# Optimization experiments

Hardware: AMD Instinct MI355X
Metric: run time of the kernel (lower is better)

The kernel has to match this reference:

```python
import jax, jax.numpy as jnp
import numpy as np

B, L, H, Q = 64, 512, 1024, 64
VA_H = 256


def setup_inputs() -> dict:
    key = jax.random.key(0)
    ks = jax.random.split(key, 10)
    hidden_states = jax.random.normal(ks[0], (B, L, H), dtype=jnp.float32)
    quad_spans = jax.random.randint(ks[1], (B, Q, 4), 0, L, dtype=jnp.int64)
    quad_mask = jnp.ones((B, Q), dtype=jnp.int32)
    s = 0.02
    W1 = jax.random.normal(ks[2], (3 * H, VA_H), dtype=jnp.float32) * s
    b1 = jnp.zeros((VA_H,), dtype=jnp.float32)
    W2 = jax.random.normal(ks[3], (VA_H, VA_H // 2), dtype=jnp.float32) * s
    b2 = jnp.zeros((VA_H // 2,), dtype=jnp.float32)
    W3 = jax.random.normal(ks[4], (VA_H // 2, 2), dtype=jnp.float32) * s
    b3 = jnp.zeros((2,), dtype=jnp.float32)
    return {"hidden_states": hidden_states, "quad_spans": quad_spans,
            "quad_mask": quad_mask, "W1": W1, "b1": b1, "W2": W2, "b2": b2,
            "W3": W3, "b3": b3}


def _pool_spans(hidden_states, quad_spans, quad_mask):
    # hidden_states [B,L,H]; quad_spans [B,Q,4]; quad_mask [B,Q]
    Bn, Ln, Hn = hidden_states.shape
    pos = jnp.arange(Ln)[None, None, :]                      # [1,1,L]
    asp_s = quad_spans[:, :, 0:1]
    asp_e = quad_spans[:, :, 1:2]
    opi_s = quad_spans[:, :, 2:3]
    opi_e = quad_spans[:, :, 3:4]
    asp_valid = asp_s >= 2
    opi_valid = opi_s >= 2
    sep = pos == 1                                           # [SEP] fallback
    asp_m = ((pos >= asp_s) & (pos <= asp_e) & asp_valid) | (~asp_valid & sep)
    opi_m = ((pos >= opi_s) & (pos <= opi_e) & opi_valid) | (~opi_valid & sep)
    qm = (quad_mask != 0)[:, :, None]
    asp_f = (asp_m & qm).astype(hidden_states.dtype)         # [B,Q,L]
    opi_f = (opi_m & qm).astype(hidden_states.dtype)
    h_asp = jnp.einsum('bql,blh->bqh', asp_f, hidden_states) / jnp.clip(
        asp_f.sum(-1, keepdims=True), 1.0, None)
    h_opi = jnp.einsum('bql,blh->bqh', opi_f, hidden_states) / jnp.clip(
        opi_f.sum(-1, keepdims=True), 1.0, None)
    return h_asp, h_opi


def reference(hidden_states, quad_spans, quad_mask, W1, b1, W2, b2, W3, b3):
    h_asp, h_opi = _pool_spans(hidden_states, quad_spans, quad_mask)
    h_pair = jnp.concatenate([h_asp, h_opi, h_asp * h_opi], axis=-1)  # [B,Q,3H]
    x = jax.nn.gelu(h_pair @ W1 + b1, approximate=False)   # torch GELU = exact
    x = jax.nn.gelu(x @ W2 + b2, approximate=False)        # dropout: eval mode
    x = x @ W3 + b3                                        # [B,Q,2]
    va = jax.nn.sigmoid(x) * 8.0 + 1.0
    return va * quad_mask[:, :, None].astype(va.dtype)
```

## Files before the change

### kernel.cpp

```cpp
#include <hip/hip_runtime.h>
#include <math.h>


typedef __attribute__((ext_vector_type(4))) float f32x4;
typedef __attribute__((ext_vector_type(8))) short bf16x8;

#define NPAIR 4096
#define LSEQ 512
#define HDIM 1024

#if defined(__has_builtin)
#if __has_builtin(__builtin_amdgcn_global_load_lds)
#define HAVE_GLDS 1
#endif
#endif
#ifndef HAVE_GLDS
#define HAVE_GLDS 0
#endif

__device__ __forceinline__ unsigned int pack2(float lo, float hi) {
  const unsigned int a = __float_as_uint(lo) + 0x8000u;
  const unsigned int b = __float_as_uint(hi) + 0x8000u;
  return __builtin_amdgcn_perm(b, a, 0x07060302u);
}
__device__ __forceinline__ unsigned short f2bf(float f) {
  return (unsigned short)((__float_as_uint(f) + 0x8000u) >> 16);
}
__device__ __forceinline__ float gelu(float x) {
  return 0.5f * x * (1.f + erff(x * 0.70710678118654752f));
}

__global__ __launch_bounds__(256, 4) void prep_kernel(
    const float* __restrict__ hs, const int* __restrict__ spans,
    const int* __restrict__ qmask, unsigned short* __restrict__ hpair,
    const float* __restrict__ W1, unsigned short* __restrict__ W1T,
    const float* __restrict__ W2, unsigned short* __restrict__ W2T) {
  __shared__ __align__(16) unsigned char smem[34816];
  __shared__ float scl[128];
  const int tid = threadIdx.x;

  if (blockIdx.x >= 1024) {
    float(*t)[33] = (float(*)[33])smem;
    const float* in;
    unsigned short* out;
    int C, R, c0, r0;
    int blk = blockIdx.x - 1024;
    if (blk < 768) {
      in = W1; out = W1T; R = 3072; C = 256;
      c0 = (blk & 7) * 32; r0 = (blk >> 3) * 32;
    } else {
      blk -= 768;
      in = W2; out = W2T; R = 256; C = 128;
      c0 = (blk & 3) * 32; r0 = (blk >> 2) * 32;
    }
    const int x = tid & 31, y = tid >> 5;
#pragma unroll
    for (int i = 0; i < 32; i += 8)
      t[y + i][x] = in[(size_t)(r0 + y + i) * C + c0 + x];
    __syncthreads();
#pragma unroll
    for (int i = 0; i < 32; i += 8)
      out[(size_t)(c0 + y + i) * R + r0 + x] = f2bf(t[x][y + i]);
    return;
  }

  typedef unsigned short BlT[64][40];
  BlT* Bl = (BlT*)smem;
  float(*S)[68] = (float(*)[68])smem;

  const int b = blockIdx.x >> 4;
  const int n0 = (blockIdx.x & 15) * 64;
  const int lane = tid & 63;
  const int lm = lane & 15, quad = lane >> 4;
  const int wm = (tid >> 6) * 32;

  const bool is64 =
      (spans[1] == 0) && (spans[3] == 0) && (spans[5] == 0) && (spans[7] == 0);

  auto span_of = [&](int r, int& s, int& e) {
    const int q = r & 63, t = r >> 6;
    const int idx = (b * 64 + q) * 4 + t * 2;
    s = is64 ? spans[idx * 2] : spans[idx];
    e = is64 ? spans[idx * 2 + 2] : spans[idx + 1];
    if (s < 2) { s = 1; e = 1; }
  };
  int s0, e0, s1, e1;
  span_of(wm + lm, s0, e0);
  span_of(wm + 16 + lm, s1, e1);

  if (tid < 128) {
    int s, e;
    span_of(tid, s, e);
    const int c = (e >= s) ? (e - s + 1) : 0;
    const float sc = 1.f / (float)(c < 1 ? 1 : c);
    scl[tid] = (qmask[b * 64 + (tid & 63)] != 0) ? sc : 0.f;
  }

  f32x4 acc[2][4];
#pragma unroll
  for (int f = 0; f < 2; ++f)
#pragma unroll
    for (int g = 0; g < 4; ++g) acc[f][g] = f32x4{0.f, 0.f, 0.f, 0.f};

  const float* hsb = hs + (size_t)b * (LSEQ * HDIM);
  const int nl = tid & 63;
  const int kw = (tid >> 6) * 8;

  auto load8 = [&](int kbase, unsigned int (&tmp)[4]) {
    const float* src = hsb + (size_t)(kbase + kw) * HDIM + n0 + nl;
#pragma unroll
    for (int i = 0; i < 4; ++i) {
      const float f0 = src[(size_t)(2 * i) * HDIM];
      const float f1 = src[(size_t)(2 * i + 1) * HDIM];
      tmp[i] = pack2(f0, f1);
    }
  };

  unsigned int tmp[4];
  load8(0, tmp);
  *(uint4*)&Bl[0][nl][kw] = make_uint4(tmp[0], tmp[1], tmp[2], tmp[3]);

  for (int it = 0; it < 16; ++it) {
    const int k0 = it * 32;
    __syncthreads();
    if (it < 15) load8(k0 + 32, tmp);

    bf16x8 a0, a1;
#pragma unroll
    for (int j = 0; j < 8; ++j) {
      const int k = k0 + quad * 8 + j;
      a0[j] = (short)((k >= s0 && k <= e0) ? 0x3F80 : 0);
      a1[j] = (short)((k >= s1 && k <= e1) ? 0x3F80 : 0);
    }
    const BlT& Bc = Bl[it & 1];
#pragma unroll
    for (int g = 0; g < 4; ++g) {
      bf16x8 bg = *(const bf16x8*)&Bc[g * 16 + lm][quad * 8];
      acc[0][g] = __builtin_amdgcn_mfma_f32_16x16x32_bf16(a0, bg, acc[0][g], 0, 0, 0);
      acc[1][g] = __builtin_amdgcn_mfma_f32_16x16x32_bf16(a1, bg, acc[1][g], 0, 0, 0);
    }
    if (it < 15) {
      *(uint4*)&Bl[(it + 1) & 1][nl][kw] = make_uint4(tmp[0], tmp[1], tmp[2], tmp[3]);
    }
  }

  __syncthreads();
#pragma unroll
  for (int f = 0; f < 2; ++f)
#pragma unroll
    for (int g = 0; g < 4; ++g)
#pragma unroll
      for (int r = 0; r < 4; ++r)
        S[wm + f * 16 + quad * 4 + r][g * 16 + lm] = acc[f][g][r];
  __syncthreads();

  const int q = tid >> 2;
  const int cg = (tid & 3) * 16;
  const float sA = scl[q], sO = scl[64 + q];
  unsigned short* dst = hpair + (size_t)(b * 64 + q) * 3072 + n0 + cg;
#pragma unroll
  for (int h = 0; h < 2; ++h) {
    float a[8], o[8];
#pragma unroll
    for (int i = 0; i < 8; ++i) {
      a[i] = S[q][cg + h * 8 + i] * sA;
      o[i] = S[64 + q][cg + h * 8 + i] * sO;
    }
    uint4 wa, wo, wp;
    wa.x = pack2(a[0], a[1]); wa.y = pack2(a[2], a[3]);
    wa.z = pack2(a[4], a[5]); wa.w = pack2(a[6], a[7]);
    wo.x = pack2(o[0], o[1]); wo.y = pack2(o[2], o[3]);
    wo.z = pack2(o[4], o[5]); wo.w = pack2(o[6], o[7]);
    wp.x = pack2(a[0] * o[0], a[1] * o[1]); wp.y = pack2(a[2] * o[2], a[3] * o[3]);
    wp.z = pack2(a[4] * o[4], a[5] * o[5]); wp.w = pack2(a[6] * o[6], a[7] * o[7]);
    *(uint4*)(dst + h * 8) = wa;
    *(uint4*)(dst + 1024 + h * 8) = wo;
    *(uint4*)(dst + 2048 + h * 8) = wp;
  }
}

__global__ __launch_bounds__(256) void gemm_bt_64x256(
    const unsigned short* __restrict__ A, const unsigned short* __restrict__ Bt,
    float* __restrict__ P, int M, int N, int K, int KH) {
  __shared__ __align__(16) unsigned short Al[2][64][32];
  __shared__ __align__(16) unsigned short Bl[2][256][32];
  const int bm = blockIdx.x * 64;
  const int kz = blockIdx.z * KH;
  const int tid = threadIdx.x;
  const int wave = tid >> 6, lane = tid & 63;
  const int wn = wave * 64;
  const int lm = lane & 15, lk = (lane >> 4) * 8;

  const int srow = lane >> 2;
  const int scol = (lane & 3) * 8;
  const unsigned short* ga = A + (size_t)(bm + wave * 16 + srow) * K + kz + scol;
  const unsigned short* gb = Bt + (size_t)(wn + srow) * K + kz + scol;

  f32x4 acc[4][4];
#pragma unroll
  for (int i = 0; i < 4; ++i)
#pragma unroll
    for (int j = 0; j < 4; ++j) acc[i][j] = f32x4{0.f, 0.f, 0.f, 0.f};

  auto stage = [&](int u, int k0) {
#if HAVE_GLDS
    __builtin_amdgcn_global_load_lds(ga + k0, &Al[u][wave * 16][0], 16, 0, 0);
#pragma unroll
    for (int c = 0; c < 4; ++c)
      __builtin_amdgcn_global_load_lds(gb + (size_t)(c * 16) * K + k0,
                                       &Bl[u][wn + c * 16][0], 16, 0, 0);
#else
    *(uint4*)&Al[u][wave * 16 + srow][scol] = *(const uint4*)(ga + k0);
#pragma unroll
    for (int c = 0; c < 4; ++c)
      *(uint4*)&Bl[u][wn + c * 16 + srow][scol] =
          *(const uint4*)(gb + (size_t)(c * 16) * K + k0);
#endif
  };

  const int NT = KH / 32;
  stage(0, 0);
  for (int t = 0; t < NT; ++t) {
    __syncthreads();
    if (t + 1 < NT) stage((t + 1) & 1, (t + 1) * 32);
    const int u = t & 1;
    bf16x8 af[4], bf[4];
#pragma unroll
    for (int i = 0; i < 4; ++i) {
      af[i] = *(const bf16x8*)&Al[u][i * 16 + lm][lk];
      bf[i] = *(const bf16x8*)&Bl[u][wn + i * 16 + lm][lk];
    }
#pragma unroll
    for (int i = 0; i < 4; ++i)
#pragma unroll
      for (int j = 0; j < 4; ++j)
        acc[i][j] = __builtin_amdgcn_mfma_f32_16x16x32_bf16(af[i], bf[j], acc[i][j], 0, 0, 0);
  }

  float* Pz = P + (size_t)blockIdx.z * M * N;
  const int rq = (lane >> 4) << 2;
#pragma unroll
  for (int i = 0; i < 4; ++i)
#pragma unroll
    for (int j = 0; j < 4; ++j) {
      const int r0 = bm + i * 16 + rq;
      const int c0 = wn + j * 16 + lm;
#pragma unroll
      for (int r = 0; r < 4; ++r)
        Pz[(size_t)(r0 + r) * N + c0] = acc[i][j][r];
    }
}

__global__ __launch_bounds__(256) void tail_kernel(
    const float* __restrict__ P, const float* __restrict__ b1,
    const unsigned short* __restrict__ W2T, const float* __restrict__ b2,
    const float* __restrict__ W3, const float* __restrict__ b3,
    const int* __restrict__ qmask, float* __restrict__ out) {
  __shared__ __align__(16) unsigned short Al[16 * 264];
  __shared__ float S2[16][132];
  __shared__ float w3[256];

  const int m0 = blockIdx.x * 16;
  const int tid = threadIdx.x;
  const int wave = tid >> 6, lane = tid & 63;
  const int lm = lane & 15, quad = lane >> 4;
  const int wn = wave * 32;

  w3[tid] = W3[tid];

  {
    const int row = tid >> 4;
    const int slot = tid & 15;
#pragma unroll
    for (int ss = 0; ss < 2; ++ss) {
      const int s = slot + ss * 16;
      const float* pb = P + (size_t)(m0 + row) * 256 + s * 8;
      float v[8];
      {
        float4 ba = *(const float4*)(b1 + s * 8);
        float4 bb = *(const float4*)(b1 + s * 8 + 4);
        v[0] = ba.x; v[1] = ba.y; v[2] = ba.z; v[3] = ba.w;
        v[4] = bb.x; v[5] = bb.y; v[6] = bb.z; v[7] = bb.w;
      }
#pragma unroll
      for (int z = 0; z < 4; ++z) {
        const float* pz = pb + (size_t)z * ((size_t)NPAIR * 256);
        float4 a0 = *(const float4*)pz;
        float4 a1 = *(const float4*)(pz + 4);
        v[0] += a0.x; v[1] += a0.y; v[2] += a0.z; v[3] += a0.w;
        v[4] += a1.x; v[5] += a1.y; v[6] += a1.z; v[7] += a1.w;
      }
      uint4 w;
      w.x = pack2(gelu(v[0]), gelu(v[1]));
      w.y = pack2(gelu(v[2]), gelu(v[3]));
      w.z = pack2(gelu(v[4]), gelu(v[5]));
      w.w = pack2(gelu(v[6]), gelu(v[7]));
      *(uint4*)((char*)Al + (size_t)row * 528 + s * 16) = w;
    }
  }
  __syncthreads();

  f32x4 acc[2];
  acc[0] = f32x4{0.f, 0.f, 0.f, 0.f};
  acc[1] = f32x4{0.f, 0.f, 0.f, 0.f};
#pragma unroll
  for (int ks = 0; ks < 8; ++ks) {
    bf16x8 a = *(const bf16x8*)((char*)Al + (size_t)lm * 528 + ks * 64 + quad * 16);
#pragma unroll
    for (int g = 0; g < 2; ++g) {
      const int n = wn + g * 16 + lm;
      bf16x8 b = *(const bf16x8*)(W2T + (size_t)n * 256 + ks * 32 + quad * 8);
      acc[g] = __builtin_amdgcn_mfma_f32_16x16x32_bf16(a, b, acc[g], 0, 0, 0);
    }
  }

#pragma unroll
  for (int g = 0; g < 2; ++g) {
    const int col = wn + g * 16 + lm;
    const float bc = b2[col];
#pragma unroll
    for (int r = 0; r < 4; ++r) S2[quad * 4 + r][col] = gelu(acc[g][r] + bc);
  }
  __syncthreads();

  if (tid < 128) {
    const int row = tid >> 3, o = (tid >> 2) & 1, q4 = tid & 3;
    float part = 0.f;
#pragma unroll 8
    for (int c = q4; c < 128; c += 4) part += S2[row][c] * w3[c * 2 + o];
    part += __shfl_xor(part, 1);
    part += __shfl_xor(part, 2);
    if (q4 == 0) {
      const int pair = m0 + row;
      const float a = part + b3[o];
      const float qmf = (float)qmask[pair];
      out[pair * 2 + o] = ((1.f / (1.f + expf(-a))) * 8.f + 1.f) * qmf;
    }
  }
}

extern "C" void kernel_launch(void* const* d_in, const int* in_sizes, int n_in,
                              void* d_out, int out_size, void* d_ws,
                              size_t ws_size, hipStream_t stream) {
  const float* hs = (const float*)d_in[0];
  const int* spans = (const int*)d_in[1];
  const int* qmask = (const int*)d_in[2];
  const float* W1 = (const float*)d_in[3];
  const float* b1 = (const float*)d_in[4];
  const float* W2 = (const float*)d_in[5];
  const float* b2 = (const float*)d_in[6];
  const float* W3 = (const float*)d_in[7];
  const float* b3 = (const float*)d_in[8];
  float* out = (float*)d_out;

  const size_t HPAIR_B = 25165824;
  const size_t P_B = 16777216;
  const size_t W1T_B = 1572864;

  char* ws = (char*)d_ws;
  size_t off = 0;
  unsigned short* hpair = (unsigned short*)(ws + off); off += HPAIR_B;
  float* P = (float*)(ws + off);                       off += P_B;
  unsigned short* W1T = (unsigned short*)(ws + off);   off += W1T_B;
  unsigned short* W2T = (unsigned short*)(ws + off);

  prep_kernel<<<1824, 256, 0, stream>>>(hs, spans, qmask, hpair, W1, W1T, W2, W2T);
  gemm_bt_64x256<<<dim3(64, 1, 4), 256, 0, stream>>>(hpair, W1T, P, NPAIR,
                                                     256, 3072, 768);
  tail_kernel<<<256, 256, 0, stream>>>(P, b1, W2T, b2, W3, b3, qmask, out);
}
```

Baseline: 238.9 us.

## Fuse split-K GEMM and MLP tail into one kernel with atomic counters

Merges the split-K W1 GEMM and the tail MLP kernel into a single launch of 256 blocks. Each group of four K-split blocks signals completion through a per-row-tile atomic counter, which prep_kernel resets. Each block then spins until its group finishes and reduces its own 16-row slice. This removes one kernel launch and the gap between kernels. In exchange it relies on all blocks of a group being co-resident, since the spin-wait would deadlock otherwise, and adds fence and atomic overhead.

```diff
diff --git a/kernel.cpp b/kernel.cpp
--- a/kernel.cpp
+++ b/kernel.cpp
@@ -34,12 +34,14 @@
     const float* __restrict__ hs, const int* __restrict__ spans,
     const int* __restrict__ qmask, unsigned short* __restrict__ hpair,
     const float* __restrict__ W1, unsigned short* __restrict__ W1T,
-    const float* __restrict__ W2, unsigned short* __restrict__ W2T) {
+    const float* __restrict__ W2, unsigned short* __restrict__ W2T,
+    unsigned int* __restrict__ cnt) {
   __shared__ __align__(16) unsigned char smem[34816];
   __shared__ float scl[128];
   const int tid = threadIdx.x;
 
   if (blockIdx.x >= 1024) {
+    if (blockIdx.x == 1024 && tid < 64) cnt[tid] = 0;
     float(*t)[33] = (float(*)[33])smem;
     const float* in;
     unsigned short* out;
@@ -179,94 +181,111 @@
   }
 }
 
-__global__ __launch_bounds__(256) void gemm_bt_64x256(
+__global__ __launch_bounds__(256) void gemm_tail_kernel(
     const unsigned short* __restrict__ A, const unsigned short* __restrict__ Bt,
-    float* __restrict__ P, int M, int N, int K, int KH) {
-  __shared__ __align__(16) unsigned short Al[2][64][32];
-  __shared__ __align__(16) unsigned short Bl[2][256][32];
-  const int bm = blockIdx.x * 64;
-  const int kz = blockIdx.z * KH;
-  const int tid = threadIdx.x;
-  const int wave = tid >> 6, lane = tid & 63;
-  const int wn = wave * 64;
-  const int lm = lane & 15, lk = (lane >> 4) * 8;
-
-  const int srow = lane >> 2;
-  const int scol = (lane & 3) * 8;
-  const unsigned short* ga = A + (size_t)(bm + wave * 16 + srow) * K + kz + scol;
-  const unsigned short* gb = Bt + (size_t)(wn + srow) * K + kz + scol;
-
-  f32x4 acc[4][4];
-#pragma unroll
-  for (int i = 0; i < 4; ++i)
-#pragma unroll
-    for (int j = 0; j < 4; ++j) acc[i][j] = f32x4{0.f, 0.f, 0.f, 0.f};
-
-  auto stage = [&](int u, int k0) {
-#if HAVE_GLDS
-    __builtin_amdgcn_global_load_lds(ga + k0, &Al[u][wave * 16][0], 16, 0, 0);
-#pragma unroll
-    for (int c = 0; c < 4; ++c)
-      __builtin_amdgcn_global_load_lds(gb + (size_t)(c * 16) * K + k0,
-                                       &Bl[u][wn + c * 16][0], 16, 0, 0);
-#else
-    *(uint4*)&Al[u][wave * 16 + srow][scol] = *(const uint4*)(ga + k0);
-#pragma unroll
-    for (int c = 0; c < 4; ++c)
-      *(uint4*)&Bl[u][wn + c * 16 + srow][scol] =
-          *(const uint4*)(gb + (size_t)(c * 16) * K + k0);
-#endif
-  };
-
-  const int NT = KH / 32;
-  stage(0, 0);
-  for (int t = 0; t < NT; ++t) {
-    __syncthreads();
-    if (t + 1 < NT) stage((t + 1) & 1, (t + 1) * 32);
-    const int u = t & 1;
-    bf16x8 af[4], bf[4];
-#pragma unroll
-    for (int i = 0; i < 4; ++i) {
-      af[i] = *(const bf16x8*)&Al[u][i * 16 + lm][lk];
-      bf[i] = *(const bf16x8*)&Bl[u][wn + i * 16 + lm][lk];
-    }
-#pragma unroll
-    for (int i = 0; i < 4; ++i)
-#pragma unroll
-      for (int j = 0; j < 4; ++j)
-        acc[i][j] = __builtin_amdgcn_mfma_f32_16x16x32_bf16(af[i], bf[j], acc[i][j], 0, 0, 0);
-  }
-
-  float* Pz = P + (size_t)blockIdx.z * M * N;
-  const int rq = (lane >> 4) << 2;
-#pragma unroll
-  for (int i = 0; i < 4; ++i)
-#pragma unroll
-    for (int j = 0; j < 4; ++j) {
-      const int r0 = bm + i * 16 + rq;
-      const int c0 = wn + j * 16 + lm;
-#pragma unroll
-      for (int r = 0; r < 4; ++r)
-        Pz[(size_t)(r0 + r) * N + c0] = acc[i][j][r];
-    }
-}
-
-__global__ __launch_bounds__(256) void tail_kernel(
-    const float* __restrict__ P, const float* __restrict__ b1,
+    float* __restrict__ P, const float* __restrict__ b1,
     const unsigned short* __restrict__ W2T, const float* __restrict__ b2,
     const float* __restrict__ W3, const float* __restrict__ b3,
-    const int* __restrict__ qmask, float* __restrict__ out) {
-  __shared__ __align__(16) unsigned short Al[16 * 264];
-  __shared__ float S2[16][132];
-  __shared__ float w3[256];
-
-  const int m0 = blockIdx.x * 16;
+    const int* __restrict__ qmask, float* __restrict__ out,
+    unsigned int* __restrict__ cnt) {
+  __shared__ __align__(16) unsigned char smem[40960];
   const int tid = threadIdx.x;
   const int wave = tid >> 6, lane = tid & 63;
   const int lm = lane & 15, quad = lane >> 4;
-  const int wn = wave * 32;
-
+
+  const int m = blockIdx.x >> 2, z = blockIdx.x & 3;
+  const int K = 3072, N = 256, KH = 768;
+
+  {
+    typedef unsigned short AlT[64][32];
+    typedef unsigned short BlT[256][32];
+    AlT* Al = (AlT*)smem;
+    BlT* Bl = (BlT*)(smem + 8192);
+    const int bm = m * 64;
+    const int kz = z * KH;
+    const int wn = wave * 64;
+    const int lk = (lane >> 4) * 8;
+
+    const int srow = lane >> 2;
+    const int scol = (lane & 3) * 8;
+    const unsigned short* ga = A + (size_t)(bm + wave * 16 + srow) * K + kz + scol;
+    const unsigned short* gb = Bt + (size_t)(wn + srow) * K + kz + scol;
+
+    f32x4 acc[4][4];
+#pragma unroll
+    for (int i = 0; i < 4; ++i)
+#pragma unroll
+      for (int j = 0; j < 4; ++j) acc[i][j] = f32x4{0.f, 0.f, 0.f, 0.f};
+
+    auto stage = [&](int u, int k0) {
+#if HAVE_GLDS
+      __builtin_amdgcn_global_load_lds(ga + k0, &Al[u][wave * 16][0], 16, 0, 0);
+#pragma unroll
+      for (int c = 0; c < 4; ++c)
+        __builtin_amdgcn_global_load_lds(gb + (size_t)(c * 16) * K + k0,
+                                         &Bl[u][wn + c * 16][0], 16, 0, 0);
+#else
+      *(uint4*)&Al[u][wave * 16 + srow][scol] = *(const uint4*)(ga + k0);
+#pragma unroll
+      for (int c = 0; c < 4; ++c)
+        *(uint4*)&Bl[u][wn + c * 16 + srow][scol] =
+            *(const uint4*)(gb + (size_t)(c * 16) * K + k0);
+#endif
+    };
+
+    const int NT = KH / 32;
+    stage(0, 0);
+    for (int t = 0; t < NT; ++t) {
+      __syncthreads();
+      if (t + 1 < NT) stage((t + 1) & 1, (t + 1) * 32);
+      const int u = t & 1;
+      bf16x8 af[4], bf[4];
+#pragma unroll
+      for (int i = 0; i < 4; ++i) {
+        af[i] = *(const bf16x8*)&Al[u][i * 16 + lm][lk];
+        bf[i] = *(const bf16x8*)&Bl[u][wn + i * 16 + lm][lk];
+      }
+#pragma unroll
+      for (int i = 0; i < 4; ++i)
+#pragma unroll
+        for (int j = 0; j < 4; ++j)
+          acc[i][j] = __builtin_amdgcn_mfma_f32_16x16x32_bf16(af[i], bf[j], acc[i][j], 0, 0, 0);
+    }
+
+    float* Pz = P + (size_t)z * NPAIR * N;
+    const int rq = (lane >> 4) << 2;
+#pragma unroll
+    for (int i = 0; i < 4; ++i)
+#pragma unroll
+      for (int j = 0; j < 4; ++j) {
+        const int r0 = bm + i * 16 + rq;
+        const int c0 = wn + j * 16 + lm;
+#pragma unroll
+        for (int r = 0; r < 4; ++r)
+          Pz[(size_t)(r0 + r) * N + c0] = acc[i][j][r];
+      }
+  }
+
+  __threadfence();
+  __syncthreads();
+  unsigned short* Ax = (unsigned short*)smem;
+  float(*S2)[132] = (float(*)[132])(smem + 8448);
+  float* w3 = (float*)(smem + 16896);
   w3[tid] = W3[tid];
+
+  if (tid == 0) {
+    __hip_atomic_fetch_add(&cnt[m], 1u, __ATOMIC_RELEASE,
+                           __HIP_MEMORY_SCOPE_AGENT);
+    while (__hip_atomic_load(&cnt[m], __ATOMIC_ACQUIRE,
+                             __HIP_MEMORY_SCOPE_AGENT) < 4u) {
+      __builtin_amdgcn_s_sleep(8);
+    }
+  }
+  __syncthreads();
+  (void)__hip_atomic_load(&cnt[m], __ATOMIC_ACQUIRE, __HIP_MEMORY_SCOPE_AGENT);
+
+  const int m0 = blockIdx.x * 16;
+  const int wn2 = wave * 32;
 
   {
     const int row = tid >> 4;
@@ -283,8 +302,8 @@
         v[4] = bb.x; v[5] = bb.y; v[6] = bb.z; v[7] = bb.w;
       }
 #pragma unroll
-      for (int z = 0; z < 4; ++z) {
-        const float* pz = pb + (size_t)z * ((size_t)NPAIR * 256);
+      for (int zz = 0; zz < 4; ++zz) {
+        const float* pz = pb + (size_t)zz * ((size_t)NPAIR * 256);
         float4 a0 = *(const float4*)pz;
         float4 a1 = *(const float4*)(pz + 4);
         v[0] += a0.x; v[1] += a0.y; v[2] += a0.z; v[3] += a0.w;
@@ -295,31 +314,31 @@
       w.y = pack2(gelu(v[2]), gelu(v[3]));
       w.z = pack2(gelu(v[4]), gelu(v[5]));
       w.w = pack2(gelu(v[6]), gelu(v[7]));
-      *(uint4*)((char*)Al + (size_t)row * 528 + s * 16) = w;
-    }
-  }
-  __syncthreads();
-
-  f32x4 acc[2];
-  acc[0] = f32x4{0.f, 0.f, 0.f, 0.f};
-  acc[1] = f32x4{0.f, 0.f, 0.f, 0.f};
+      *(uint4*)((char*)Ax + (size_t)row * 528 + s * 16) = w;
+    }
+  }
+  __syncthreads();
+
+  f32x4 acc2[2];
+  acc2[0] = f32x4{0.f, 0.f, 0.f, 0.f};
+  acc2[1] = f32x4{0.f, 0.f, 0.f, 0.f};
 #pragma unroll
   for (int ks = 0; ks < 8; ++ks) {
-    bf16x8 a = *(const bf16x8*)((char*)Al + (size_t)lm * 528 + ks * 64 + quad * 16);
+    bf16x8 a = *(const bf16x8*)((char*)Ax + (size_t)lm * 528 + ks * 64 + quad * 16);
 #pragma unroll
     for (int g = 0; g < 2; ++g) {
-      const int n = wn + g * 16 + lm;
+      const int n = wn2 + g * 16 + lm;
       bf16x8 b = *(const bf16x8*)(W2T + (size_t)n * 256 + ks * 32 + quad * 8);
-      acc[g] = __builtin_amdgcn_mfma_f32_16x16x32_bf16(a, b, acc[g], 0, 0, 0);
+      acc2[g] = __builtin_amdgcn_mfma_f32_16x16x32_bf16(a, b, acc2[g], 0, 0, 0);
     }
   }
 
 #pragma unroll
   for (int g = 0; g < 2; ++g) {
-    const int col = wn + g * 16 + lm;
+    const int col = wn2 + g * 16 + lm;
     const float bc = b2[col];
 #pragma unroll
-    for (int r = 0; r < 4; ++r) S2[quad * 4 + r][col] = gelu(acc[g][r] + bc);
+    for (int r = 0; r < 4; ++r) S2[quad * 4 + r][col] = gelu(acc2[g][r] + bc);
   }
   __syncthreads();
 
@@ -356,16 +375,18 @@
   const size_t HPAIR_B = 25165824;
   const size_t P_B = 16777216;
   const size_t W1T_B = 1572864;
+  const size_t W2T_B = 65536;
 
   char* ws = (char*)d_ws;
   size_t off = 0;
   unsigned short* hpair = (unsigned short*)(ws + off); off += HPAIR_B;
   float* P = (float*)(ws + off);                       off += P_B;
   unsigned short* W1T = (unsigned short*)(ws + off);   off += W1T_B;
-  unsigned short* W2T = (unsigned short*)(ws + off);
-
-  prep_kernel<<<1824, 256, 0, stream>>>(hs, spans, qmask, hpair, W1, W1T, W2, W2T);
-  gemm_bt_64x256<<<dim3(64, 1, 4), 256, 0, stream>>>(hpair, W1T, P, NPAIR,
-                                                     256, 3072, 768);
-  tail_kernel<<<256, 256, 0, stream>>>(P, b1, W2T, b2, W3, b3, qmask, out);
-}
+  unsigned short* W2T = (unsigned short*)(ws + off);   off += W2T_B;
+  unsigned int* cnt = (unsigned int*)(ws + off);
+
+  prep_kernel<<<1824, 256, 0, stream>>>(hs, spans, qmask, hpair, W1, W1T, W2,
+                                        W2T, cnt);
+  gemm_tail_kernel<<<256, 256, 0, stream>>>(hpair, W1T, P, b1, W2T, b2, W3,
+                                            b3, qmask, out, cnt);
+}
```

Result: slower. 270.9 us (+13.4%).

## Fuse first-layer GEMM into MLP tail kernel, drop split-K partial buffer

Applied to the files above, without the earlier changes.

Replaces the split-K LDS-staged W1 GEMM and the separate tail kernel with one kernel. Each 512-thread block computes 16 rows across all 256 hidden columns, loading A and W1T fragments straight from global memory into registers, then applies GELU and runs the W2/W3 stages in the same block. This removes the 16 MB fp32 partial-sum buffer, its write and read-back, and one launch. The cost is no LDS reuse: every wave reloads the same A rows, and W1T is read by all 256 blocks, so only 256 blocks stream the full K=3072 with less reuse than the tiled GEMM.

```diff
diff --git a/kernel.cpp b/kernel.cpp
--- a/kernel.cpp
+++ b/kernel.cpp
@@ -8,15 +8,6 @@
 #define NPAIR 4096
 #define LSEQ 512
 #define HDIM 1024
-
-#if defined(__has_builtin)
-#if __has_builtin(__builtin_amdgcn_global_load_lds)
-#define HAVE_GLDS 1
-#endif
-#endif
-#ifndef HAVE_GLDS
-#define HAVE_GLDS 0
-#endif
 
 __device__ __forceinline__ unsigned int pack2(float lo, float hi) {
   const unsigned int a = __float_as_uint(lo) + 0x8000u;
@@ -179,147 +170,74 @@
   }
 }
 
-__global__ __launch_bounds__(256) void gemm_bt_64x256(
-    const unsigned short* __restrict__ A, const unsigned short* __restrict__ Bt,
-    float* __restrict__ P, int M, int N, int K, int KH) {
-  __shared__ __align__(16) unsigned short Al[2][64][32];
-  __shared__ __align__(16) unsigned short Bl[2][256][32];
-  const int bm = blockIdx.x * 64;
-  const int kz = blockIdx.z * KH;
-  const int tid = threadIdx.x;
-  const int wave = tid >> 6, lane = tid & 63;
-  const int wn = wave * 64;
-  const int lm = lane & 15, lk = (lane >> 4) * 8;
-
-  const int srow = lane >> 2;
-  const int scol = (lane & 3) * 8;
-  const unsigned short* ga = A + (size_t)(bm + wave * 16 + srow) * K + kz + scol;
-  const unsigned short* gb = Bt + (size_t)(wn + srow) * K + kz + scol;
-
-  f32x4 acc[4][4];
-#pragma unroll
-  for (int i = 0; i < 4; ++i)
-#pragma unroll
-    for (int j = 0; j < 4; ++j) acc[i][j] = f32x4{0.f, 0.f, 0.f, 0.f};
-
-  auto stage = [&](int u, int k0) {
-#if HAVE_GLDS
-    __builtin_amdgcn_global_load_lds(ga + k0, &Al[u][wave * 16][0], 16, 0, 0);
-#pragma unroll
-    for (int c = 0; c < 4; ++c)
-      __builtin_amdgcn_global_load_lds(gb + (size_t)(c * 16) * K + k0,
-                                       &Bl[u][wn + c * 16][0], 16, 0, 0);
-#else
-    *(uint4*)&Al[u][wave * 16 + srow][scol] = *(const uint4*)(ga + k0);
-#pragma unroll
-    for (int c = 0; c < 4; ++c)
-      *(uint4*)&Bl[u][wn + c * 16 + srow][scol] =
-          *(const uint4*)(gb + (size_t)(c * 16) * K + k0);
-#endif
-  };
-
-  const int NT = KH / 32;
-  stage(0, 0);
-  for (int t = 0; t < NT; ++t) {
-    __syncthreads();
-    if (t + 1 < NT) stage((t + 1) & 1, (t + 1) * 32);
-    const int u = t & 1;
-    bf16x8 af[4], bf[4];
-#pragma unroll
-    for (int i = 0; i < 4; ++i) {
-      af[i] = *(const bf16x8*)&Al[u][i * 16 + lm][lk];
-      bf[i] = *(const bf16x8*)&Bl[u][wn + i * 16 + lm][lk];
-    }
-#pragma unroll
-    for (int i = 0; i < 4; ++i)
-#pragma unroll
-      for (int j = 0; j < 4; ++j)
-        acc[i][j] = __builtin_amdgcn_mfma_f32_16x16x32_bf16(af[i], bf[j], acc[i][j], 0, 0, 0);
-  }
-
-  float* Pz = P + (size_t)blockIdx.z * M * N;
-  const int rq = (lane >> 4) << 2;
-#pragma unroll
-  for (int i = 0; i < 4; ++i)
-#pragma unroll
-    for (int j = 0; j < 4; ++j) {
-      const int r0 = bm + i * 16 + rq;
-      const int c0 = wn + j * 16 + lm;
-#pragma unroll
-      for (int r = 0; r < 4; ++r)
-        Pz[(size_t)(r0 + r) * N + c0] = acc[i][j][r];
-    }
-}
-
-__global__ __launch_bounds__(256) void tail_kernel(
-    const float* __restrict__ P, const float* __restrict__ b1,
-    const unsigned short* __restrict__ W2T, const float* __restrict__ b2,
-    const float* __restrict__ W3, const float* __restrict__ b3,
-    const int* __restrict__ qmask, float* __restrict__ out) {
-  __shared__ __align__(16) unsigned short Al[16 * 264];
+__global__ __launch_bounds__(512) void mlp_kernel(
+    const unsigned short* __restrict__ A, const unsigned short* __restrict__ W1T,
+    const float* __restrict__ b1, const unsigned short* __restrict__ W2T,
+    const float* __restrict__ b2, const float* __restrict__ W3,
+    const float* __restrict__ b3, const int* __restrict__ qmask,
+    float* __restrict__ out) {
+  __shared__ __align__(16) unsigned short x1[16 * 264];
   __shared__ float S2[16][132];
   __shared__ float w3[256];
 
-  const int m0 = blockIdx.x * 16;
+  const int bm = blockIdx.x * 16;
   const int tid = threadIdx.x;
   const int wave = tid >> 6, lane = tid & 63;
   const int lm = lane & 15, quad = lane >> 4;
-  const int wn = wave * 32;
-
-  w3[tid] = W3[tid];
+
+  if (tid < 256) w3[tid] = W3[tid];
+
+  const int wn1 = wave * 32;
+  const unsigned short* pa = A + (size_t)(bm + lm) * 3072 + quad * 8;
+  const unsigned short* pb0 = W1T + (size_t)(wn1 + lm) * 3072 + quad * 8;
+  const unsigned short* pb1 = W1T + (size_t)(wn1 + 16 + lm) * 3072 + quad * 8;
+
+  f32x4 acc1[2];
+  acc1[0] = f32x4{0.f, 0.f, 0.f, 0.f};
+  acc1[1] = f32x4{0.f, 0.f, 0.f, 0.f};
+
+  for (int kb = 0; kb < 3072; kb += 256) {
+    bf16x8 av[8], b0v[8], b1v[8];
+#pragma unroll
+    for (int s = 0; s < 8; ++s) {
+      const int k0 = kb + s * 32;
+      av[s] = *(const bf16x8*)(pa + k0);
+      b0v[s] = *(const bf16x8*)(pb0 + k0);
+      b1v[s] = *(const bf16x8*)(pb1 + k0);
+    }
+#pragma unroll
+    for (int s = 0; s < 8; ++s) {
+      acc1[0] = __builtin_amdgcn_mfma_f32_16x16x32_bf16(av[s], b0v[s], acc1[0], 0, 0, 0);
+      acc1[1] = __builtin_amdgcn_mfma_f32_16x16x32_bf16(av[s], b1v[s], acc1[1], 0, 0, 0);
+    }
+  }
+
+#pragma unroll
+  for (int g = 0; g < 2; ++g) {
+    const int n = wn1 + g * 16 + lm;
+    const float bc = b1[n];
+#pragma unroll
+    for (int r = 0; r < 4; ++r) {
+      x1[(quad * 4 + r) * 264 + n] = f2bf(gelu(acc1[g][r] + bc));
+    }
+  }
+  __syncthreads();
+
+  const int wn2 = wave * 16;
+  f32x4 acc2 = f32x4{0.f, 0.f, 0.f, 0.f};
+  const unsigned short* pw2 = W2T + (size_t)(wn2 + lm) * 256 + quad * 8;
+#pragma unroll
+  for (int ks = 0; ks < 8; ++ks) {
+    bf16x8 a = *(const bf16x8*)&x1[lm * 264 + ks * 32 + quad * 8];
+    bf16x8 b = *(const bf16x8*)(pw2 + ks * 32);
+    acc2 = __builtin_amdgcn_mfma_f32_16x16x32_bf16(a, b, acc2, 0, 0, 0);
+  }
 
   {
-    const int row = tid >> 4;
-    const int slot = tid & 15;
-#pragma unroll
-    for (int ss = 0; ss < 2; ++ss) {
-      const int s = slot + ss * 16;
-      const float* pb = P + (size_t)(m0 + row) * 256 + s * 8;
-      float v[8];
-      {
-        float4 ba = *(const float4*)(b1 + s * 8);
-        float4 bb = *(const float4*)(b1 + s * 8 + 4);
-        v[0] = ba.x; v[1] = ba.y; v[2] = ba.z; v[3] = ba.w;
-        v[4] = bb.x; v[5] = bb.y; v[6] = bb.z; v[7] = bb.w;
-      }
-#pragma unroll
-      for (int z = 0; z < 4; ++z) {
-        const float* pz = pb + (size_t)z * ((size_t)NPAIR * 256);
-        float4 a0 = *(const float4*)pz;
-        float4 a1 = *(const float4*)(pz + 4);
-        v[0] += a0.x; v[1] += a0.y; v[2] += a0.z; v[3] += a0.w;
-        v[4] += a1.x; v[5] += a1.y; v[6] += a1.z; v[7] += a1.w;
-      }
-      uint4 w;
-      w.x = pack2(gelu(v[0]), gelu(v[1]));
-      w.y = pack2(gelu(v[2]), gelu(v[3]));
-      w.z = pack2(gelu(v[4]), gelu(v[5]));
-      w.w = pack2(gelu(v[6]), gelu(v[7]));
-      *(uint4*)((char*)Al + (size_t)row * 528 + s * 16) = w;
-    }
-  }
-  __syncthreads();
-
-  f32x4 acc[2];
-  acc[0] = f32x4{0.f, 0.f, 0.f, 0.f};
-  acc[1] = f32x4{0.f, 0.f, 0.f, 0.f};
-#pragma unroll
-  for (int ks = 0; ks < 8; ++ks) {
-    bf16x8 a = *(const bf16x8*)((char*)Al + (size_t)lm * 528 + ks * 64 + quad * 16);
-#pragma unroll
-    for (int g = 0; g < 2; ++g) {
-      const int n = wn + g * 16 + lm;
-      bf16x8 b = *(const bf16x8*)(W2T + (size_t)n * 256 + ks * 32 + quad * 8);
-      acc[g] = __builtin_amdgcn_mfma_f32_16x16x32_bf16(a, b, acc[g], 0, 0, 0);
-    }
-  }
-
-#pragma unroll
-  for (int g = 0; g < 2; ++g) {
-    const int col = wn + g * 16 + lm;
+    const int col = wn2 + lm;
     const float bc = b2[col];
 #pragma unroll
-    for (int r = 0; r < 4; ++r) S2[quad * 4 + r][col] = gelu(acc[g][r] + bc);
+    for (int r = 0; r < 4; ++r) S2[quad * 4 + r][col] = gelu(acc2[r] + bc);
   }
   __syncthreads();
 
@@ -331,7 +249,7 @@
     part += __shfl_xor(part, 1);
     part += __shfl_xor(part, 2);
     if (q4 == 0) {
-      const int pair = m0 + row;
+      const int pair = bm + row;
       const float a = part + b3[o];
       const float qmf = (float)qmask[pair];
       out[pair * 2 + o] = ((1.f / (1.f + expf(-a))) * 8.f + 1.f) * qmf;
@@ -354,18 +272,14 @@
   float* out = (float*)d_out;
 
   const size_t HPAIR_B = 25165824;
-  const size_t P_B = 16777216;
   const size_t W1T_B = 1572864;
 
   char* ws = (char*)d_ws;
   size_t off = 0;
   unsigned short* hpair = (unsigned short*)(ws + off); off += HPAIR_B;
-  float* P = (float*)(ws + off);                       off += P_B;
   unsigned short* W1T = (unsigned short*)(ws + off);   off += W1T_B;
   unsigned short* W2T = (unsigned short*)(ws + off);
 
   prep_kernel<<<1824, 256, 0, stream>>>(hs, spans, qmask, hpair, W1, W1T, W2, W2T);
-  gemm_bt_64x256<<<dim3(64, 1, 4), 256, 0, stream>>>(hpair, W1T, P, NPAIR,
-                                                     256, 3072, 768);
-  tail_kernel<<<256, 256, 0, stream>>>(P, b1, W2T, b2, W3, b3, qmask, out);
-}
+  mlp_kernel<<<256, 512, 0, stream>>>(hpair, W1T, b1, W2T, b2, W3, b3, qmask, out);
+}
```

Result: slower. 277.9 us (+16.3%).
